# Optimization experiments

Hardware: AMD Instinct MI355X
Metric: run time of the kernel (lower is better)

Reference implementation:

```python
import jax, jax.numpy as jnp
import numpy as np

NUM_TABLES = 10
EMB_DIM = 3
VOCAB = 1_000_000
N_IDX = 4_000_000
N_BAGS = 100_000


def setup_inputs() -> dict:
    key = jax.random.key(0)
    k_idx, k_off, k_w = jax.random.split(key, 3)
    eb_input = jax.random.randint(k_idx, (N_IDX,), 0, VOCAB, dtype=jnp.int64)
    # EmbeddingBag offsets: sorted, first element must be 0, values in [0, N_IDX)
    eb_offset = jnp.sort(jax.random.randint(k_off, (N_BAGS,), 0, N_IDX, dtype=jnp.int64))
    eb_offset = eb_offset.at[0].set(0)
    # torch.nn.EmbeddingBag default init: N(0, 1)
    W = jax.random.normal(k_w, (NUM_TABLES, VOCAB, EMB_DIM), dtype=jnp.float32)
    return {"eb_input": eb_input, "eb_offset": eb_offset, "W": W}


def _bag_sums(eb_input, eb_offset, W):
    # segment id for each index position: bag b covers [offset[b], offset[b+1])
    n = eb_input.shape[0]
    seg = jnp.searchsorted(eb_offset, jnp.arange(n), side="right") - 1  # [N]
    gathered = W[:, eb_input, :]  # [T, N, D] irregular gather
    # sum-pool per bag for every table
    per_bag = jax.vmap(lambda g: jax.ops.segment_sum(g, seg, num_segments=eb_offset.shape[0]))(gathered)  # [T, B, D]
    return per_bag


def reference(eb_input, eb_offset, W):
    per_bag = _bag_sums(eb_input, eb_offset, W)  # [10, B, 3]
    outs = [per_bag[i] for i in range(NUM_TABLES)]
    outs[5] = jnp.sum(outs[5], axis=1, keepdims=True)  # [B, 1]
    outs[6] = jnp.sum(outs[6], axis=1, keepdims=True)  # [B, 1]
    cat = jnp.concatenate(outs, axis=1)  # [B, 26]
    return jnp.sum(cat, axis=0)  # [26]
```

## Files before the change

kernel.cpp:

```cpp
#include <hip/hip_runtime.h>

#define VOCAB 1000000
#define NUM_TABLES 10
#define OUT_SIZE 26
#define BUCKET_BITS 12
#define BPB 4096
#define NBUCKETS 245
#define CHUNK 4096
#define MAXSRC 1024
#define RBLOCKS_PER_TABLE 256
#define NRBLK (NUM_TABLES * RBLOCKS_PER_TABLE)
#define RTHREADS 256


__global__ void __launch_bounds__(256) scatter_kernel(
    const int* __restrict__ idx, int n,
    unsigned short* __restrict__ scat,
    unsigned int* __restrict__ gs32)
{
    __shared__ unsigned int lcount[256];
    __shared__ unsigned int sc[256];
    __shared__ unsigned short stage[CHUNK];
    const int tid = threadIdx.x;
    lcount[tid] = 0u;
    __syncthreads();

    const int4* idx4 = (const int4*)idx;
    const int n4 = n >> 2;
    const int base4 = blockIdx.x * (CHUNK / 4);
    int4 q[4];
    bool val[4];
    unsigned rank[16];
    unsigned bkt[16];
#pragma unroll
    for (int j = 0; j < 4; ++j) {
        int i4 = base4 + j * 256 + tid;
        val[j] = (i4 < n4);
        if (val[j]) q[j] = idx4[i4];
    }
#pragma unroll
    for (int j = 0; j < 4; ++j) {
        if (val[j]) {
            unsigned v[4] = {(unsigned)q[j].x, (unsigned)q[j].y, (unsigned)q[j].z, (unsigned)q[j].w};
#pragma unroll
            for (int e = 0; e < 4; ++e) {
                bkt[j * 4 + e] = v[e] >> BUCKET_BITS;
                rank[j * 4 + e] = atomicAdd(&lcount[bkt[j * 4 + e]], 1u);
            }
        }
    }
    unsigned trank[3], tbkt[3];
    int tcnt = 0;
    if (blockIdx.x == gridDim.x - 1 && tid == 0) {
        for (int i = n4 * 4; i < n; ++i) {
            unsigned u = (unsigned)idx[i];
            tbkt[tcnt] = u >> BUCKET_BITS;
            trank[tcnt] = atomicAdd(&lcount[tbkt[tcnt]], 1u);
            ++tcnt;
        }
    }
    __syncthreads();
    unsigned cnt = (tid < NBUCKETS) ? lcount[tid] : 0u;
    sc[tid] = cnt;
    __syncthreads();
#pragma unroll
    for (int off = 1; off < 256; off <<= 1) {
        unsigned v = sc[tid];
        unsigned a = (tid >= off) ? sc[tid - off] : 0u;
        __syncthreads();
        sc[tid] = v + a;
        __syncthreads();
    }
    unsigned excl = sc[tid] - cnt;
    if (tid < NBUCKETS) gs32[tid * MAXSRC + blockIdx.x] = excl | (cnt << 16);
    lcount[tid] = excl;
    __syncthreads();
#pragma unroll
    for (int j = 0; j < 4; ++j) {
        if (val[j]) {
            unsigned v[4] = {(unsigned)q[j].x, (unsigned)q[j].y, (unsigned)q[j].z, (unsigned)q[j].w};
#pragma unroll
            for (int e = 0; e < 4; ++e) {
                unsigned k = j * 4 + e;
                stage[lcount[bkt[k]] + rank[k]] = (unsigned short)(v[e] & (BPB - 1));
            }
        }
    }
    if (blockIdx.x == gridDim.x - 1 && tid == 0) {
        for (int i = 0; i < tcnt; ++i) {
            unsigned u = (unsigned)idx[n4 * 4 + i];
            stage[lcount[tbkt[i]] + trank[i]] = (unsigned short)(u & (BPB - 1));
        }
    }
    __syncthreads();
    uint4* dst = (uint4*)(scat + (size_t)blockIdx.x * CHUNK);
    const uint4* src = (const uint4*)stage;
#pragma unroll
    for (int j = 0; j < 2; ++j) dst[j * 256 + tid] = src[j * 256 + tid];
}

__global__ void __launch_bounds__(1024) bucket_hist_kernel(
    const unsigned short* __restrict__ scat,
    const unsigned int* __restrict__ gs32, int nsrc,
    unsigned int* __restrict__ hist)
{
    __shared__ unsigned int h[BPB];
    const int b = blockIdx.x;
    const int tid = threadIdx.x;
    for (int i = tid; i < BPB; i += 1024) h[i] = 0u;
    __syncthreads();
    if (tid < nsrc) {
        unsigned g32 = gs32[b * MAXSRC + tid];
        unsigned s = g32 & 0xffffu, c = g32 >> 16;
        const unsigned short* p = scat + (size_t)tid * CHUNK + s;
        unsigned k = 0;
        for (; k + 4 <= c; k += 4) {
            unsigned short a0 = p[k], a1 = p[k + 1], a2 = p[k + 2], a3 = p[k + 3];
            atomicAdd(&h[a0], 1u);
            atomicAdd(&h[a1], 1u);
            atomicAdd(&h[a2], 1u);
            atomicAdd(&h[a3], 1u);
        }
        for (; k < c; ++k) atomicAdd(&h[p[k]], 1u);
    }
    __syncthreads();
    int nb4 = min(BPB, VOCAB - b * BPB) >> 2;
    uint4* dst = (uint4*)(hist + (size_t)b * BPB);
    const uint4* src = (const uint4*)h;
    if (tid < nb4) dst[tid] = src[tid];
}

__device__ inline float wave_reduce(float v) {
#pragma unroll
    for (int o = 32; o > 0; o >>= 1) v += __shfl_down(v, o, 64);
    return v;
}

__global__ void __launch_bounds__(RTHREADS) reduce_kernel(const float* __restrict__ W,
                                                          const unsigned int* __restrict__ hist,
                                                          float* __restrict__ partials) {
    const int t = blockIdx.x / RBLOCKS_PER_TABLE;
    const int b = blockIdx.x % RBLOCKS_PER_TABLE;
    const float4* __restrict__ W4 = (const float4*)(W + (size_t)t * VOCAB * 3);
    const uint4* __restrict__ h4 = (const uint4*)hist;
    const int ngroups = VOCAB / 4;
    float a0 = 0.f, a1 = 0.f, a2 = 0.f;
    const int stride = RBLOCKS_PER_TABLE * RTHREADS;
    for (int g = b * RTHREADS + (int)threadIdx.x; g < ngroups; g += stride) {
        uint4 c4 = h4[g];
        float4 w0 = W4[3 * g + 0];
        float4 w1 = W4[3 * g + 1];
        float4 w2 = W4[3 * g + 2];
        float c0 = (float)c4.x, c1 = (float)c4.y, c2 = (float)c4.z, c3 = (float)c4.w;
        a0 += c0 * w0.x + c1 * w0.w + c2 * w1.z + c3 * w2.y;
        a1 += c0 * w0.y + c1 * w1.x + c2 * w1.w + c3 * w2.z;
        a2 += c0 * w0.z + c1 * w1.y + c2 * w2.x + c3 * w2.w;
    }
    a0 = wave_reduce(a0);
    a1 = wave_reduce(a1);
    a2 = wave_reduce(a2);
    __shared__ float s[3][4];
    int wave = threadIdx.x >> 6;
    int lane = threadIdx.x & 63;
    if (lane == 0) { s[0][wave] = a0; s[1][wave] = a1; s[2][wave] = a2; }
    __syncthreads();
    if (threadIdx.x == 0) {
        partials[0 * NRBLK + blockIdx.x] = s[0][0] + s[0][1] + s[0][2] + s[0][3];
        partials[1 * NRBLK + blockIdx.x] = s[1][0] + s[1][1] + s[1][2] + s[1][3];
        partials[2 * NRBLK + blockIdx.x] = s[2][0] + s[2][1] + s[2][2] + s[2][3];
    }
}

__global__ void __launch_bounds__(1024) final_kernel(const float* __restrict__ partials,
                                                     float* __restrict__ out) {
    __shared__ float ts[32];
    const int tid = threadIdx.x;
    const int srs = tid >> 5;
    const int j = tid & 31;
    float v = 0.f;
    if (srs < 30) {
        const int t = srs / 3, d = srs % 3;
        const float* p = partials + (size_t)d * NRBLK + t * RBLOCKS_PER_TABLE;
#pragma unroll
        for (int k = 0; k < RBLOCKS_PER_TABLE / 32; ++k) v += p[k * 32 + j];
    }
#pragma unroll
    for (int off = 16; off > 0; off >>= 1) v += __shfl_down(v, off);
    if (j == 0 && srs < 30) ts[srs] = v;
    __syncthreads();
    if (tid < OUT_SIZE) {
        float r;
        if (tid < 15) r = ts[tid];
        else if (tid == 15) r = ts[15] + ts[16] + ts[17];
        else if (tid == 16) r = ts[18] + ts[19] + ts[20];
        else r = ts[tid + 4];
        out[tid] = r;
    }
}


__global__ void zero_kernel_fb(unsigned int* __restrict__ hist, float* __restrict__ out) {
    int i = blockIdx.x * blockDim.x + threadIdx.x;
    int n4 = VOCAB / 4;
    if (i < n4) ((uint4*)hist)[i] = make_uint4(0u, 0u, 0u, 0u);
    if (i < OUT_SIZE) out[i] = 0.0f;
}

__global__ void hist_kernel_fb(const int* __restrict__ idx, unsigned int* __restrict__ hist, int n) {
    int i = blockIdx.x * blockDim.x + threadIdx.x;
    int i4 = i * 4;
    if (i4 + 3 < n) {
        int4 v = ((const int4*)idx)[i];
        atomicAdd(&hist[v.x], 1u);
        atomicAdd(&hist[v.y], 1u);
        atomicAdd(&hist[v.z], 1u);
        atomicAdd(&hist[v.w], 1u);
    } else {
        for (int j = i4; j < n; ++j) atomicAdd(&hist[idx[j]], 1u);
    }
}

__global__ void __launch_bounds__(RTHREADS) reduce_kernel_fb(const float* __restrict__ W,
                                                             const unsigned int* __restrict__ hist,
                                                             float* __restrict__ out) {
    const int t = blockIdx.x / 64;
    const int b = blockIdx.x % 64;
    const float4* __restrict__ W4 = (const float4*)(W + (size_t)t * VOCAB * 3);
    const uint4* __restrict__ h4 = (const uint4*)hist;
    const int ngroups = VOCAB / 4;
    float a0 = 0.f, a1 = 0.f, a2 = 0.f;
    const int stride = 64 * RTHREADS;
    for (int g = b * RTHREADS + (int)threadIdx.x; g < ngroups; g += stride) {
        uint4 c4 = h4[g];
        float4 w0 = W4[3 * g + 0];
        float4 w1 = W4[3 * g + 1];
        float4 w2 = W4[3 * g + 2];
        float c0 = (float)c4.x, c1 = (float)c4.y, c2 = (float)c4.z, c3 = (float)c4.w;
        a0 += c0 * w0.x + c1 * w0.w + c2 * w1.z + c3 * w2.y;
        a1 += c0 * w0.y + c1 * w1.x + c2 * w1.w + c3 * w2.z;
        a2 += c0 * w0.z + c1 * w1.y + c2 * w2.x + c3 * w2.w;
    }
    a0 = wave_reduce(a0);
    a1 = wave_reduce(a1);
    a2 = wave_reduce(a2);
    __shared__ float s[3][4];
    int wave = threadIdx.x >> 6;
    int lane = threadIdx.x & 63;
    if (lane == 0) { s[0][wave] = a0; s[1][wave] = a1; s[2][wave] = a2; }
    __syncthreads();
    if (threadIdx.x == 0) {
        float r0 = s[0][0] + s[0][1] + s[0][2] + s[0][3];
        float r1 = s[1][0] + s[1][1] + s[1][2] + s[1][3];
        float r2 = s[2][0] + s[2][1] + s[2][2] + s[2][3];
        if (t == 5) atomicAdd(&out[15], r0 + r1 + r2);
        else if (t == 6) atomicAdd(&out[16], r0 + r1 + r2);
        else {
            int base = (t < 5) ? t * 3 : 17 + (t - 7) * 3;
            atomicAdd(&out[base + 0], r0);
            atomicAdd(&out[base + 1], r1);
            atomicAdd(&out[base + 2], r2);
        }
    }
}


extern "C" void kernel_launch(void* const* d_in, const int* in_sizes, int n_in,
                              void* d_out, int out_size, void* d_ws, size_t ws_size,
                              hipStream_t stream) {
    const int* eb_input = (const int*)d_in[0];
    const float* W = (const float*)d_in[2];
    float* out = (float*)d_out;
    int n_idx = in_sizes[0];

    const int nsrc = (n_idx + CHUNK - 1) / CHUNK;
    const size_t scat_bytes = (size_t)MAXSRC * CHUNK * 2;
    const size_t gs_off = scat_bytes;
    const size_t gs_bytes = (size_t)NBUCKETS * MAXSRC * 4;
    const size_t hist_off = gs_off + gs_bytes;
    const size_t hist_bytes = (size_t)VOCAB * 4;
    const size_t part_off = (hist_off + hist_bytes + 255) & ~(size_t)255;
    const size_t need = part_off + (size_t)3 * NRBLK * 4;

    if (nsrc <= MAXSRC && ws_size >= need) {
        unsigned short* scat = (unsigned short*)d_ws;
        unsigned int* gs32 = (unsigned int*)((char*)d_ws + gs_off);
        unsigned int* hist = (unsigned int*)((char*)d_ws + hist_off);
        float* partials = (float*)((char*)d_ws + part_off);

        scatter_kernel<<<nsrc, 256, 0, stream>>>(eb_input, n_idx, scat, gs32);
        bucket_hist_kernel<<<NBUCKETS, 1024, 0, stream>>>(scat, gs32, nsrc, hist);
        reduce_kernel<<<NRBLK, RTHREADS, 0, stream>>>(W, hist, partials);
        final_kernel<<<1, 1024, 0, stream>>>(partials, out);
    } else {
        unsigned int* hist = (unsigned int*)d_ws;
        int zblocks = (VOCAB / 4 + 255) / 256;
        zero_kernel_fb<<<zblocks, 256, 0, stream>>>(hist, out);
        int hthreads = (n_idx + 3) / 4;
        int hblocks = (hthreads + 255) / 256;
        hist_kernel_fb<<<hblocks, 256, 0, stream>>>(eb_input, hist, n_idx);
        reduce_kernel_fb<<<NUM_TABLES * 64, RTHREADS, 0, stream>>>(W, hist, out);
    }
}
```

Baseline: 208.5 us.

## Fuse bucket histogram with weighted table reduction, dropping global histogram

The per-bucket histogram kernel now multiplies its shared-memory counts directly against all ten embedding tables and writes per-bucket partial sums, so the separate reduce kernel and the global histogram array are removed. This saves writing and rereading a vocabulary-sized count array and one kernel launch. The bucket-offset table is also transposed so the scatter kernel writes rows contiguously. In exchange, the reduction of W now runs on only 245 blocks of 1024 threads, each issuing 30 float4 loads and holding 30 accumulators, so memory-level parallelism and occupancy for streaming the 120MB of W may drop.

```diff
diff --git a/kernel.cpp b/kernel.cpp
--- a/kernel.cpp
+++ b/kernel.cpp
@@ -8,9 +8,9 @@
 #define NBUCKETS 245
 #define CHUNK 4096
 #define MAXSRC 1024
-#define RBLOCKS_PER_TABLE 256
-#define NRBLK (NUM_TABLES * RBLOCKS_PER_TABLE)
-#define RTHREADS 256
+#define GSTRIDE 256
+#define NPB NBUCKETS
+#define NSERIES 30
 
 
 __global__ void __launch_bounds__(256) scatter_kernel(
@@ -20,7 +20,7 @@
 {
     __shared__ unsigned int lcount[256];
     __shared__ unsigned int sc[256];
-    __shared__ unsigned short stage[CHUNK];
+    __shared__ __align__(16) unsigned short stage[CHUNK];
     const int tid = threadIdx.x;
     lcount[tid] = 0u;
     __syncthreads();
@@ -72,7 +72,7 @@
         __syncthreads();
     }
     unsigned excl = sc[tid] - cnt;
-    if (tid < NBUCKETS) gs32[tid * MAXSRC + blockIdx.x] = excl | (cnt << 16);
+    if (tid < NBUCKETS) gs32[(size_t)blockIdx.x * GSTRIDE + tid] = excl | (cnt << 16);
     lcount[tid] = excl;
     __syncthreads();
 #pragma unroll
@@ -99,18 +99,26 @@
     for (int j = 0; j < 2; ++j) dst[j * 256 + tid] = src[j * 256 + tid];
 }
 
-__global__ void __launch_bounds__(1024) bucket_hist_kernel(
+__device__ inline float wave_reduce(float v) {
+#pragma unroll
+    for (int o = 32; o > 0; o >>= 1) v += __shfl_down(v, o, 64);
+    return v;
+}
+
+__global__ void __launch_bounds__(1024) bucket_reduce_kernel(
     const unsigned short* __restrict__ scat,
     const unsigned int* __restrict__ gs32, int nsrc,
-    unsigned int* __restrict__ hist)
+    const float* __restrict__ W,
+    float* __restrict__ partials)
 {
-    __shared__ unsigned int h[BPB];
+    __shared__ __align__(16) unsigned int h[BPB];
+    __shared__ float sm[16][NSERIES];
     const int b = blockIdx.x;
     const int tid = threadIdx.x;
     for (int i = tid; i < BPB; i += 1024) h[i] = 0u;
     __syncthreads();
     if (tid < nsrc) {
-        unsigned g32 = gs32[b * MAXSRC + tid];
+        unsigned g32 = gs32[(size_t)tid * GSTRIDE + b];
         unsigned s = g32 & 0xffffu, c = g32 >> 16;
         const unsigned short* p = scat + (size_t)tid * CHUNK + s;
         unsigned k = 0;
@@ -124,50 +132,43 @@
         for (; k < c; ++k) atomicAdd(&h[p[k]], 1u);
     }
     __syncthreads();
-    int nb4 = min(BPB, VOCAB - b * BPB) >> 2;
-    uint4* dst = (uint4*)(hist + (size_t)b * BPB);
-    const uint4* src = (const uint4*)h;
-    if (tid < nb4) dst[tid] = src[tid];
-}
-
-__device__ inline float wave_reduce(float v) {
-#pragma unroll
-    for (int o = 32; o > 0; o >>= 1) v += __shfl_down(v, o, 64);
-    return v;
-}
-
-__global__ void __launch_bounds__(RTHREADS) reduce_kernel(const float* __restrict__ W,
-                                                          const unsigned int* __restrict__ hist,
-                                                          float* __restrict__ partials) {
-    const int t = blockIdx.x / RBLOCKS_PER_TABLE;
-    const int b = blockIdx.x % RBLOCKS_PER_TABLE;
-    const float4* __restrict__ W4 = (const float4*)(W + (size_t)t * VOCAB * 3);
-    const uint4* __restrict__ h4 = (const uint4*)hist;
-    const int ngroups = VOCAB / 4;
-    float a0 = 0.f, a1 = 0.f, a2 = 0.f;
-    const int stride = RBLOCKS_PER_TABLE * RTHREADS;
-    for (int g = b * RTHREADS + (int)threadIdx.x; g < ngroups; g += stride) {
-        uint4 c4 = h4[g];
-        float4 w0 = W4[3 * g + 0];
-        float4 w1 = W4[3 * g + 1];
-        float4 w2 = W4[3 * g + 2];
+
+    const int nbg = min(BPB, VOCAB - b * BPB) >> 2;
+    float acc[NUM_TABLES][3];
+#pragma unroll
+    for (int t = 0; t < NUM_TABLES; ++t) {
+        acc[t][0] = 0.f; acc[t][1] = 0.f; acc[t][2] = 0.f;
+    }
+    if (tid < nbg) {
+        uint4 c4 = ((const uint4*)h)[tid];
         float c0 = (float)c4.x, c1 = (float)c4.y, c2 = (float)c4.z, c3 = (float)c4.w;
-        a0 += c0 * w0.x + c1 * w0.w + c2 * w1.z + c3 * w2.y;
-        a1 += c0 * w0.y + c1 * w1.x + c2 * w1.w + c3 * w2.z;
-        a2 += c0 * w0.z + c1 * w1.y + c2 * w2.x + c3 * w2.w;
-    }
-    a0 = wave_reduce(a0);
-    a1 = wave_reduce(a1);
-    a2 = wave_reduce(a2);
-    __shared__ float s[3][4];
-    int wave = threadIdx.x >> 6;
-    int lane = threadIdx.x & 63;
-    if (lane == 0) { s[0][wave] = a0; s[1][wave] = a1; s[2][wave] = a2; }
-    __syncthreads();
-    if (threadIdx.x == 0) {
-        partials[0 * NRBLK + blockIdx.x] = s[0][0] + s[0][1] + s[0][2] + s[0][3];
-        partials[1 * NRBLK + blockIdx.x] = s[1][0] + s[1][1] + s[1][2] + s[1][3];
-        partials[2 * NRBLK + blockIdx.x] = s[2][0] + s[2][1] + s[2][2] + s[2][3];
+        const int g = b * (BPB / 4) + tid;
+#pragma unroll
+        for (int t = 0; t < NUM_TABLES; ++t) {
+            const float4* __restrict__ W4 = (const float4*)(W + (size_t)t * VOCAB * 3);
+            float4 w0 = W4[3 * g + 0];
+            float4 w1 = W4[3 * g + 1];
+            float4 w2 = W4[3 * g + 2];
+            acc[t][0] += c0 * w0.x + c1 * w0.w + c2 * w1.z + c3 * w2.y;
+            acc[t][1] += c0 * w0.y + c1 * w1.x + c2 * w1.w + c3 * w2.z;
+            acc[t][2] += c0 * w0.z + c1 * w1.y + c2 * w2.x + c3 * w2.w;
+        }
+    }
+    const int wave = tid >> 6, lane = tid & 63;
+#pragma unroll
+    for (int t = 0; t < NUM_TABLES; ++t) {
+#pragma unroll
+        for (int d = 0; d < 3; ++d) {
+            float v = wave_reduce(acc[t][d]);
+            if (lane == 0) sm[wave][t * 3 + d] = v;
+        }
+    }
+    __syncthreads();
+    if (tid < NSERIES) {
+        float v = 0.f;
+#pragma unroll
+        for (int w = 0; w < 16; ++w) v += sm[w][tid];
+        partials[(size_t)tid * NPB + b] = v;
     }
 }
 
@@ -178,15 +179,17 @@
     const int srs = tid >> 5;
     const int j = tid & 31;
     float v = 0.f;
-    if (srs < 30) {
-        const int t = srs / 3, d = srs % 3;
-        const float* p = partials + (size_t)d * NRBLK + t * RBLOCKS_PER_TABLE;
-#pragma unroll
-        for (int k = 0; k < RBLOCKS_PER_TABLE / 32; ++k) v += p[k * 32 + j];
+    if (srs < NSERIES) {
+        const float* p = partials + (size_t)srs * NPB;
+#pragma unroll
+        for (int k = 0; k < 8; ++k) {
+            int i = k * 32 + j;
+            if (i < NPB) v += p[i];
+        }
     }
 #pragma unroll
     for (int off = 16; off > 0; off >>= 1) v += __shfl_down(v, off);
-    if (j == 0 && srs < 30) ts[srs] = v;
+    if (j == 0 && srs < NSERIES) ts[srs] = v;
     __syncthreads();
     if (tid < OUT_SIZE) {
         float r;
@@ -219,6 +222,8 @@
         for (int j = i4; j < n; ++j) atomicAdd(&hist[idx[j]], 1u);
     }
 }
+
+#define RTHREADS 256
 
 __global__ void __launch_bounds__(RTHREADS) reduce_kernel_fb(const float* __restrict__ W,
                                                              const unsigned int* __restrict__ hist,
@@ -275,21 +280,17 @@
     const int nsrc = (n_idx + CHUNK - 1) / CHUNK;
     const size_t scat_bytes = (size_t)MAXSRC * CHUNK * 2;
     const size_t gs_off = scat_bytes;
-    const size_t gs_bytes = (size_t)NBUCKETS * MAXSRC * 4;
-    const size_t hist_off = gs_off + gs_bytes;
-    const size_t hist_bytes = (size_t)VOCAB * 4;
-    const size_t part_off = (hist_off + hist_bytes + 255) & ~(size_t)255;
-    const size_t need = part_off + (size_t)3 * NRBLK * 4;
+    const size_t gs_bytes = (size_t)MAXSRC * GSTRIDE * 4;
+    const size_t part_off = (gs_off + gs_bytes + 255) & ~(size_t)255;
+    const size_t need = part_off + (size_t)NSERIES * NPB * 4;
 
     if (nsrc <= MAXSRC && ws_size >= need) {
         unsigned short* scat = (unsigned short*)d_ws;
         unsigned int* gs32 = (unsigned int*)((char*)d_ws + gs_off);
-        unsigned int* hist = (unsigned int*)((char*)d_ws + hist_off);
         float* partials = (float*)((char*)d_ws + part_off);
 
         scatter_kernel<<<nsrc, 256, 0, stream>>>(eb_input, n_idx, scat, gs32);
-        bucket_hist_kernel<<<NBUCKETS, 1024, 0, stream>>>(scat, gs32, nsrc, hist);
-        reduce_kernel<<<NRBLK, RTHREADS, 0, stream>>>(W, hist, partials);
+        bucket_reduce_kernel<<<NBUCKETS, 1024, 0, stream>>>(scat, gs32, nsrc, W, partials);
         final_kernel<<<1, 1024, 0, stream>>>(partials, out);
     } else {
         unsigned int* hist = (unsigned int*)d_ws;
```

New measurement: 214.7 us. 3.0% more time.

## Enlarge scatter chunks and spread bucket histogram reads across waves and lanes

Applied to the files above, without the earlier changes.

The scatter kernel now uses 1024-thread blocks covering 16K indices each, cutting the number of source chunks from about 1000 to about 245. The bucket histogram kernel stops giving each thread one whole source segment to walk serially. Instead each wave takes a source segment and its 64 lanes read it in a strided, coalesced way. The per-source segment descriptors are transposed to a source-major layout. The goal is to remove the serial, uncoalesced per-thread loop in the histogram stage, at the cost of more threads idling during the 256-entry scan in the scatter kernel.

```diff
diff --git a/kernel.cpp b/kernel.cpp
--- a/kernel.cpp
+++ b/kernel.cpp
@@ -6,23 +6,24 @@
 #define BUCKET_BITS 12
 #define BPB 4096
 #define NBUCKETS 245
-#define CHUNK 4096
-#define MAXSRC 1024
+#define CHUNK 16384
+#define MAXSRC 256
+#define GSTRIDE 256
 #define RBLOCKS_PER_TABLE 256
 #define NRBLK (NUM_TABLES * RBLOCKS_PER_TABLE)
 #define RTHREADS 256
 
 
-__global__ void __launch_bounds__(256) scatter_kernel(
+__global__ void __launch_bounds__(1024) scatter_kernel(
     const int* __restrict__ idx, int n,
     unsigned short* __restrict__ scat,
     unsigned int* __restrict__ gs32)
 {
     __shared__ unsigned int lcount[256];
     __shared__ unsigned int sc[256];
-    __shared__ unsigned short stage[CHUNK];
+    __shared__ __align__(16) unsigned short stage[CHUNK];
     const int tid = threadIdx.x;
-    lcount[tid] = 0u;
+    if (tid < 256) lcount[tid] = 0u;
     __syncthreads();
 
     const int4* idx4 = (const int4*)idx;
@@ -34,7 +35,7 @@
     unsigned bkt[16];
 #pragma unroll
     for (int j = 0; j < 4; ++j) {
-        int i4 = base4 + j * 256 + tid;
+        int i4 = base4 + j * 1024 + tid;
         val[j] = (i4 < n4);
         if (val[j]) q[j] = idx4[i4];
     }
@@ -60,20 +61,28 @@
         }
     }
     __syncthreads();
-    unsigned cnt = (tid < NBUCKETS) ? lcount[tid] : 0u;
-    sc[tid] = cnt;
+    unsigned cnt = 0;
+    if (tid < 256) {
+        cnt = (tid < NBUCKETS) ? lcount[tid] : 0u;
+        sc[tid] = cnt;
+    }
     __syncthreads();
 #pragma unroll
     for (int off = 1; off < 256; off <<= 1) {
-        unsigned v = sc[tid];
-        unsigned a = (tid >= off) ? sc[tid - off] : 0u;
+        unsigned v = 0, a = 0;
+        if (tid < 256) {
+            v = sc[tid];
+            if (tid >= off) a = sc[tid - off];
+        }
         __syncthreads();
-        sc[tid] = v + a;
+        if (tid < 256) sc[tid] = v + a;
         __syncthreads();
     }
-    unsigned excl = sc[tid] - cnt;
-    if (tid < NBUCKETS) gs32[tid * MAXSRC + blockIdx.x] = excl | (cnt << 16);
-    lcount[tid] = excl;
+    if (tid < 256) {
+        unsigned excl = sc[tid] - cnt;
+        if (tid < NBUCKETS) gs32[(size_t)blockIdx.x * GSTRIDE + tid] = excl | (cnt << 16);
+        lcount[tid] = excl;
+    }
     __syncthreads();
 #pragma unroll
     for (int j = 0; j < 4; ++j) {
@@ -96,7 +105,7 @@
     uint4* dst = (uint4*)(scat + (size_t)blockIdx.x * CHUNK);
     const uint4* src = (const uint4*)stage;
 #pragma unroll
-    for (int j = 0; j < 2; ++j) dst[j * 256 + tid] = src[j * 256 + tid];
+    for (int j = 0; j < 2; ++j) dst[j * 1024 + tid] = src[j * 1024 + tid];
 }
 
 __global__ void __launch_bounds__(1024) bucket_hist_kernel(
@@ -104,24 +113,18 @@
     const unsigned int* __restrict__ gs32, int nsrc,
     unsigned int* __restrict__ hist)
 {
-    __shared__ unsigned int h[BPB];
+    __shared__ __align__(16) unsigned int h[BPB];
     const int b = blockIdx.x;
     const int tid = threadIdx.x;
-    for (int i = tid; i < BPB; i += 1024) h[i] = 0u;
-    __syncthreads();
-    if (tid < nsrc) {
-        unsigned g32 = gs32[b * MAXSRC + tid];
-        unsigned s = g32 & 0xffffu, c = g32 >> 16;
-        const unsigned short* p = scat + (size_t)tid * CHUNK + s;
-        unsigned k = 0;
-        for (; k + 4 <= c; k += 4) {
-            unsigned short a0 = p[k], a1 = p[k + 1], a2 = p[k + 2], a3 = p[k + 3];
-            atomicAdd(&h[a0], 1u);
-            atomicAdd(&h[a1], 1u);
-            atomicAdd(&h[a2], 1u);
-            atomicAdd(&h[a3], 1u);
-        }
-        for (; k < c; ++k) atomicAdd(&h[p[k]], 1u);
+    const int wave = tid >> 6, lane = tid & 63;
+    ((uint4*)h)[tid] = make_uint4(0u, 0u, 0u, 0u);
+    __syncthreads();
+    for (int s = wave; s < nsrc; s += 16) {
+        unsigned g32 = gs32[(size_t)s * GSTRIDE + b];
+        unsigned st = g32 & 0xffffu, c = g32 >> 16;
+        const unsigned short* p = scat + (size_t)s * CHUNK + st;
+        for (unsigned k = lane; k < c; k += 64)
+            atomicAdd(&h[p[k]], 1u);
     }
     __syncthreads();
     int nb4 = min(BPB, VOCAB - b * BPB) >> 2;
@@ -275,7 +278,7 @@
     const int nsrc = (n_idx + CHUNK - 1) / CHUNK;
     const size_t scat_bytes = (size_t)MAXSRC * CHUNK * 2;
     const size_t gs_off = scat_bytes;
-    const size_t gs_bytes = (size_t)NBUCKETS * MAXSRC * 4;
+    const size_t gs_bytes = (size_t)MAXSRC * GSTRIDE * 4;
     const size_t hist_off = gs_off + gs_bytes;
     const size_t hist_bytes = (size_t)VOCAB * 4;
     const size_t part_off = (hist_off + hist_bytes + 255) & ~(size_t)255;
@@ -287,7 +290,7 @@
         unsigned int* hist = (unsigned int*)((char*)d_ws + hist_off);
         float* partials = (float*)((char*)d_ws + part_off);
 
-        scatter_kernel<<<nsrc, 256, 0, stream>>>(eb_input, n_idx, scat, gs32);
+        scatter_kernel<<<nsrc, 1024, 0, stream>>>(eb_input, n_idx, scat, gs32);
         bucket_hist_kernel<<<NBUCKETS, 1024, 0, stream>>>(scat, gs32, nsrc, hist);
         reduce_kernel<<<NRBLK, RTHREADS, 0, stream>>>(W, hist, partials);
         final_kernel<<<1, 1024, 0, stream>>>(partials, out);
```

Result: no change. 207.7 us (-0.4%).
